# Optimization experiments

Measured on AMD Instinct MI355X. Metric: run time of the kernel, lower is better.

## Reference

```python
import jax, jax.numpy as jnp
import numpy as np

N_HEAD = 16

def setup_inputs() -> dict:
    key = jax.random.key(0)
    ks = jax.random.split(key, 5)
    B, S, D = 4, 2048, 1024
    return {
        "string": jax.random.normal(ks[0], (B, S, D), dtype=jnp.float32),
        "string_len": jax.random.randint(ks[1], (B,), 1, S + 1),
        "Wqkv": jax.random.normal(ks[2], (D, 3 * D), dtype=jnp.float32) * 0.02,
        "bqkv": jnp.zeros((3 * D,), dtype=jnp.float32),
        "Wo": jax.random.normal(ks[3], (D, D), dtype=jnp.float32) * 0.02,
        "bo": jnp.zeros((D,), dtype=jnp.float32),
    }


def reference(string, string_len, Wqkv, bqkv, Wo, bo):
    B, S, D = string.shape
    H = N_HEAD
    hd = D // H
    x = string @ Wqkv + bqkv                      # [B,S,3D]
    q, k, v = jnp.split(x, 3, axis=-1)
    # split heads -> [B,H,S,hd]
    q = q.reshape(B, S, H, hd).transpose(0, 2, 1, 3)
    k = k.reshape(B, S, H, hd).transpose(0, 2, 1, 3)
    v = v.reshape(B, S, H, hd).transpose(0, 2, 1, 3)
    w = jnp.einsum('bhqd,bhkd->bhqk', q, k) / jnp.sqrt(jnp.float32(hd))
    causal = jnp.tril(jnp.ones((S, S), dtype=bool))  # [S,S]
    w = jnp.where(causal[None, None], w, jnp.float32(-1e9))
    w = jax.nn.softmax(w, axis=-1)
    a = jnp.einsum('bhqk,bhkd->bhqd', w, v)       # [B,H,S,hd]
    a = a.transpose(0, 2, 1, 3).reshape(B, S, D)  # merge heads
    a = a @ Wo + bo
    return a, string_len
```

## Files before the change

### kernel.cpp

```cpp
#include <hip/hip_runtime.h>
#include <stdint.h>

typedef __attribute__((ext_vector_type(8))) short bf16x8;
typedef __attribute__((ext_vector_type(4))) float f32x4;
typedef __attribute__((ext_vector_type(16))) float f32x16;
typedef __attribute__((ext_vector_type(4))) unsigned short u16x4;

static constexpr int Bn = 4, Sn = 2048, Dn = 1024, Hn = 16, HD = 64;
static constexpr int Mrows = Bn * Sn;
static constexpr int D3 = 3 * Dn;

__device__ __forceinline__ unsigned short f2bf(float f) {
  unsigned int u = __float_as_uint(f);
  u += 0x7FFF + ((u >> 16) & 1);
  return (unsigned short)(u >> 16);
}

__device__ __forceinline__ void gload16(const void* gptr, void* lptr) {
  __builtin_amdgcn_global_load_lds(
      (__attribute__((address_space(1))) void*)gptr,
      (__attribute__((address_space(3))) void*)lptr, 16, 0, 0);
}

__device__ __forceinline__ int swz8(int r) { return (r ^ (r >> 3)) & 7; }
__device__ __forceinline__ int swz4(int r) { return (r ^ (r >> 2)) & 3; }

__device__ __forceinline__ float vexp2(float x) {
#if __has_builtin(__builtin_amdgcn_exp2f)
  return __builtin_amdgcn_exp2f(x);
#else
  return exp2f(x);
#endif
}

__device__ __forceinline__ unsigned cvtpk(float lo, float hi) {
  unsigned r;
  asm("v_cvt_pk_bf16_f32 %0, %1, %2" : "=v"(r) : "v"(lo), "v"(hi));
  return r;
}

__device__ __forceinline__ float lanepull(float v, int srclane) {
  return __int_as_float(__builtin_amdgcn_ds_bpermute(srclane * 4, __float_as_int(v)));
}

__global__ void cvt_f32_bf16(const float* __restrict__ in,
                             unsigned short* __restrict__ out, int n) {
  int i = (blockIdx.x * blockDim.x + threadIdx.x) * 4;
  if (i < n) {
    const float4 v = *(const float4*)(in + i);
    u16x4 o;
    o.x = f2bf(v.x); o.y = f2bf(v.y); o.z = f2bf(v.z); o.w = f2bf(v.w);
    *(u16x4*)(out + i) = o;
  }
}

__global__ void transpose_cvt(const float* __restrict__ W,
                              unsigned short* __restrict__ Wt, int K, int N) {
  __shared__ float tile[32][33];
  const int n0 = blockIdx.x * 32, k0 = blockIdx.y * 32;
  const int tx = threadIdx.x, ty = threadIdx.y;
  #pragma unroll
  for (int j = 0; j < 4; j++)
    tile[ty + 8 * j][tx] = W[(size_t)(k0 + ty + 8 * j) * N + n0 + tx];
  __syncthreads();
  #pragma unroll
  for (int j = 0; j < 4; j++)
    Wt[(size_t)(n0 + ty + 8 * j) * K + k0 + tx] = f2bf(tile[tx][ty + 8 * j]);
}

template<bool BF16_OUT>
__global__ __launch_bounds__(256, 2)
void gemm_bt(const unsigned short* __restrict__ A,
             const unsigned short* __restrict__ Bt,
             const float* __restrict__ bias,
             void* __restrict__ Cout, int Mt, int Nt, int Kt) {
  __shared__ __align__(16) unsigned short ldsA[128 * 32];
  __shared__ __align__(16) unsigned short ldsB[128 * 32];
  const int tid  = threadIdx.x;
  const int w    = tid >> 6;
  const int lane = tid & 63;
  const int wr = w >> 1, wc = w & 1;
  const int lrow = lane & 15, lk = lane >> 4;
  const long brow = (long)blockIdx.x * 128;
  const long bcol = (long)blockIdx.y * 128;

  f32x4 acc[4][4] = {};

  const int srow_w = w * 16 + (lane >> 2);
  const int sslot  = lane & 3;

  for (int k0 = 0; k0 < Kt; k0 += 32) {
    __syncthreads();
    #pragma unroll
    for (int i = 0; i < 2; i++) {
      const int r  = i * 64 + srow_w;
      const int ca = sslot ^ swz4(r);
      gload16(A  + (size_t)(brow + r) * Kt + k0 + ca * 8, ldsA + i * 2048 + w * 512);
      gload16(Bt + (size_t)(bcol + r) * Kt + k0 + ca * 8, ldsB + i * 2048 + w * 512);
    }
    __syncthreads();
    bf16x8 af[4], bfv[4];
    #pragma unroll
    for (int mt = 0; mt < 4; mt++) {
      const int rr = wr * 64 + mt * 16 + lrow;
      af[mt] = *(const bf16x8*)(ldsA + rr * 32 + ((lk ^ swz4(rr)) * 8));
    }
    #pragma unroll
    for (int nt = 0; nt < 4; nt++) {
      const int rr = wc * 64 + nt * 16 + lrow;
      bfv[nt] = *(const bf16x8*)(ldsB + rr * 32 + ((lk ^ swz4(rr)) * 8));
    }
    #pragma unroll
    for (int mt = 0; mt < 4; mt++)
      #pragma unroll
      for (int nt = 0; nt < 4; nt++)
        acc[mt][nt] = __builtin_amdgcn_mfma_f32_16x16x32_bf16(af[mt], bfv[nt], acc[mt][nt], 0, 0, 0);
  }

  #pragma unroll
  for (int nt = 0; nt < 4; nt++) {
    const long col = bcol + wc * 64 + nt * 16 + lrow;
    const float bv = bias[col];
    #pragma unroll
    for (int mt = 0; mt < 4; mt++) {
      #pragma unroll
      for (int r = 0; r < 4; r++) {
        const long row = brow + wr * 64 + mt * 16 + lk * 4 + r;
        const float v = acc[mt][nt][r] + bv;
        if (BF16_OUT)
          ((unsigned short*)Cout)[row * Nt + col] = f2bf(v);
        else
          ((float*)Cout)[row * Nt + col] = v;
      }
    }
  }
}

__global__ __launch_bounds__(512, 2)
void attn_fwd2(const unsigned short* __restrict__ QKV,
               unsigned short* __restrict__ Out) {
  __shared__ __align__(128) unsigned char smem[65536];
  const int tid  = threadIdx.x;
  const int w    = tid >> 6;
  const int lane = tid & 63;
  const int li = lane & 31, hi = lane >> 5;
  const int bh = blockIdx.x;
  const int b  = bh >> 4, h = bh & 15;
  const int pb = blockIdx.y;
  const int qs = (w < 4) ? (63 - 4 * pb - w) : (4 * pb + (w - 4));
  const int wq = qs * 32;
  const int qrow = wq + li;

  bf16x8 qf[4];
  {
    const unsigned short* qp = QKV + (size_t)(b * Sn + qrow) * D3 + h * HD + hi * 8;
    #pragma unroll
    for (int ks = 0; ks < 4; ks++) qf[ks] = *(const bf16x8*)(qp + ks * 16);
  }

  f32x16 o0 = {}, o1 = {};
  float m = -3.0e38f, lsum = 0.f;
  const float cexp = 0.18033688011112042f;

  auto kstage = [&](int kb, unsigned char* Kb) {
    #pragma unroll
    for (int i = 0; i < 2; i++) {
      const int r    = w * 16 + i * 8 + (lane >> 3);
      const int slot = (lane & 7) ^ swz8(r);
      gload16(QKV + (size_t)(b * Sn + kb + r) * D3 + Dn + h * HD + slot * 8,
              Kb + w * 2048 + i * 1024);
    }
  };
  const int vkv8 = tid >> 3;
  const int vd0  = (tid & 7) * 8;
  auto vload = [&](int kb, int i) -> bf16x8 {
    return *(const bf16x8*)(QKV + (size_t)(b * Sn + kb + i * 64 + vkv8) * D3 + 2 * Dn + h * HD + vd0);
  };
  auto vwrite = [&](bf16x8 vv, int i, unsigned char* Vb) {
    const int kv = i * 64 + vkv8;
    #pragma unroll
    for (int j = 0; j < 8; j++) {
      const int d  = vd0 + j;
      const int vs = (d ^ (d >> 3)) & 15;
      *(unsigned short*)(Vb + d * 256 + (((kv >> 3) ^ vs) << 4) + (kv & 7) * 2) = (unsigned short)vv[j];
    }
  };

  auto substep = [&](int s, int kb, const unsigned char* Kb, const unsigned char* Vb) {
    f32x16 s0 = {}, s1 = {};
    const int r0 = s * 64 + li, r1 = s * 64 + 32 + li;
    __builtin_amdgcn_s_setprio(1);
    #pragma unroll
    for (int ks = 0; ks < 4; ks++) {
      const int slot = ks * 2 + hi;
      const bf16x8 k0 = *(const bf16x8*)(Kb + r0 * 128 + ((slot ^ swz8(r0)) * 16));
      const bf16x8 k1 = *(const bf16x8*)(Kb + r1 * 128 + ((slot ^ swz8(r1)) * 16));
      s0 = __builtin_amdgcn_mfma_f32_32x32x16_bf16(k0, qf[ks], s0, 0, 0, 0);
      s1 = __builtin_amdgcn_mfma_f32_32x32x16_bf16(k1, qf[ks], s1, 0, 0, 0);
    }
    __builtin_amdgcn_s_setprio(0);
    const int kbase = kb + s * 64;
    if (kbase + 63 > wq) {
      #pragma unroll
      for (int r = 0; r < 16; r++) {
        const int kvl = (r & 3) + 8 * (r >> 2) + 4 * hi;
        if (kbase + kvl > qrow)      s0[r] = -3.0e38f;
        if (kbase + 32 + kvl > qrow) s1[r] = -3.0e38f;
      }
    }
    float t8[8];
    #pragma unroll
    for (int r = 0; r < 8; r++)
      t8[r] = fmaxf(fmaxf(s0[r], s0[r + 8]), fmaxf(s1[r], s1[r + 8]));
    float tmax = fmaxf(fmaxf(fmaxf(t8[0], t8[1]), fmaxf(t8[2], t8[3])),
                       fmaxf(fmaxf(t8[4], t8[5]), fmaxf(t8[6], t8[7])));
    tmax = fmaxf(tmax, __shfl_xor(tmax, 32));
    if (__any(tmax > m + 44.0f)) {
      const float mn   = fmaxf(m, tmax);
      const float corr = vexp2((m - mn) * cexp);
      m = mn;
      lsum *= corr;
      #pragma unroll
      for (int r = 0; r < 16; r++) {
        const float cr = lanepull(corr, (r & 3) + 8 * (r >> 2) + 4 * hi);
        o0[r] *= cr; o1[r] *= cr;
      }
    }
    const float mc = m * cexp;
    f32x16 p0, p1;
    float psa = 0.f, psb = 0.f, psc = 0.f, psd = 0.f;
    #pragma unroll
    for (int r = 0; r < 16; r += 4) {
      p0[r] = vexp2(fmaf(s0[r], cexp, -mc));         psa += p0[r];
      p0[r + 1] = vexp2(fmaf(s0[r + 1], cexp, -mc)); psb += p0[r + 1];
      p0[r + 2] = vexp2(fmaf(s0[r + 2], cexp, -mc)); psc += p0[r + 2];
      p0[r + 3] = vexp2(fmaf(s0[r + 3], cexp, -mc)); psd += p0[r + 3];
    }
    #pragma unroll
    for (int r = 0; r < 16; r += 4) {
      p1[r] = vexp2(fmaf(s1[r], cexp, -mc));         psa += p1[r];
      p1[r + 1] = vexp2(fmaf(s1[r + 1], cexp, -mc)); psb += p1[r + 1];
      p1[r + 2] = vexp2(fmaf(s1[r + 2], cexp, -mc)); psc += p1[r + 2];
      p1[r + 3] = vexp2(fmaf(s1[r + 3], cexp, -mc)); psd += p1[r + 3];
    }
    lsum += (psa + psb) + (psc + psd);

    auto mk_pa = [&](const f32x16& pp, int base) -> bf16x8 {
      const unsigned a0 = cvtpk(pp[base + 0], pp[base + 1]);
      const unsigned a1 = cvtpk(pp[base + 2], pp[base + 3]);
      const unsigned b0 = cvtpk(pp[base + 4], pp[base + 5]);
      const unsigned b1 = cvtpk(pp[base + 6], pp[base + 7]);
      const unsigned xa0 = __shfl_xor(a0, 32), xa1 = __shfl_xor(a1, 32);
      const unsigned xb0 = __shfl_xor(b0, 32), xb1 = __shfl_xor(b1, 32);
      union { unsigned u[4]; bf16x8 v; } pu;
      pu.u[0] = hi ? xb0 : a0;
      pu.u[1] = hi ? xb1 : a1;
      pu.u[2] = hi ? b0  : xa0;
      pu.u[3] = hi ? b1  : xa1;
      return pu.v;
    };
    bf16x8 pa[4];
    pa[0] = mk_pa(p0, 0); pa[1] = mk_pa(p0, 8);
    pa[2] = mk_pa(p1, 0); pa[3] = mk_pa(p1, 8);

    const int vs0 = (li ^ (li >> 3)) & 15;
    const int vs1 = ((32 + li) ^ ((32 + li) >> 3)) & 15;
    __builtin_amdgcn_s_setprio(1);
    #pragma unroll
    for (int k16 = 0; k16 < 4; k16++) {
      const int slot = s * 8 + k16 * 2 + hi;
      const bf16x8 vb0 = *(const bf16x8*)(Vb + li * 256 + ((slot ^ vs0) << 4));
      const bf16x8 vb1 = *(const bf16x8*)(Vb + (32 + li) * 256 + ((slot ^ vs1) << 4));
      o0 = __builtin_amdgcn_mfma_f32_32x32x16_bf16(pa[k16], vb0, o0, 0, 0, 0);
      o1 = __builtin_amdgcn_mfma_f32_32x32x16_bf16(pa[k16], vb1, o1, 0, 0, 0);
    }
    __builtin_amdgcn_s_setprio(0);
  };

  kstage(0, smem);
  {
    bf16x8 va = vload(0, 0), vb = vload(0, 1);
    vwrite(va, 0, smem + 16384);
    vwrite(vb, 1, smem + 16384);
  }
  asm volatile("s_waitcnt lgkmcnt(0)");
  __builtin_amdgcn_sched_barrier(0);

  const int qsH = 63 - 4 * pb;
  const int nt  = ((qsH * 32 + 31) >> 7) + 1;
  for (int t = 0; t < nt; t++) {
    const int kb  = t << 7;
    const int cur = t & 1;
    unsigned char* Kb = smem + cur * 32768;
    unsigned char* Vb = Kb + 16384;
    const bool pre = (t + 1 < nt);
    bf16x8 vna, vnb;

    __builtin_amdgcn_s_barrier();
    if (pre) {
      kstage(kb + 128, smem + (cur ^ 1) * 32768);
      vna = vload(kb + 128, 0);
      vnb = vload(kb + 128, 1);
    }

    if (kb <= wq + 31) {
      substep(0, kb, Kb, Vb);
      if (kb + 64 <= wq + 31) substep(1, kb, Kb, Vb);
    }

    if (pre) {
      unsigned char* Vn = smem + (cur ^ 1) * 32768 + 16384;
      vwrite(vna, 0, Vn);
      vwrite(vnb, 1, Vn);
    }
    asm volatile("s_waitcnt lgkmcnt(0)");
    __builtin_amdgcn_sched_barrier(0);
  }

  const float lt = lsum + __shfl_xor(lsum, 32);
  const float rl = __builtin_amdgcn_rcpf(lt);
  #pragma unroll
  for (int r = 0; r < 16; r++) {
    const int q = (r & 3) + 8 * (r >> 2) + 4 * hi;
    const float rr = lanepull(rl, q);
    unsigned short* op = Out + (size_t)(b * Sn + wq + q) * Dn + h * HD;
    op[li]      = f2bf(o0[r] * rr);
    op[32 + li] = f2bf(o1[r] * rr);
  }
}

__global__ void copy_len(const int* __restrict__ slen, float* __restrict__ dst, int n) {
  const int i = threadIdx.x;
  if (i < n) dst[i] = (float)slen[i];
}

extern "C" void kernel_launch(void* const* d_in, const int* in_sizes, int n_in,
                              void* d_out, int out_size, void* d_ws, size_t ws_size,
                              hipStream_t stream) {
  const float* X    = (const float*)d_in[0];
  const int*   slen = (const int*)d_in[1];
  const float* Wqkv = (const float*)d_in[2];
  const float* bqkv = (const float*)d_in[3];
  const float* Wo   = (const float*)d_in[4];
  const float* bo   = (const float*)d_in[5];
  float* out = (float*)d_out;

  char* ws = (char*)d_ws;
  unsigned short* Xb    = (unsigned short*)ws;
  unsigned short* Wtq   = (unsigned short*)(ws + 16777216);
  unsigned short* Wto   = (unsigned short*)(ws + 16777216 + 6291456);
  unsigned short* QKVb  = (unsigned short*)(ws + 16777216 + 6291456 + 2097152);
  unsigned short* Attnb = Xb;

  cvt_f32_bf16<<<dim3(8192), dim3(256), 0, stream>>>(X, Xb, Mrows * Dn);
  transpose_cvt<<<dim3(96, 32), dim3(32, 8), 0, stream>>>(Wqkv, Wtq, Dn, D3);
  transpose_cvt<<<dim3(32, 32), dim3(32, 8), 0, stream>>>(Wo, Wto, Dn, Dn);

  gemm_bt<true><<<dim3(64, 24), dim3(256), 0, stream>>>(Xb, Wtq, bqkv, (void*)QKVb, Mrows, D3, Dn);
  attn_fwd2<<<dim3(64, 8), dim3(512), 0, stream>>>(QKVb, Attnb);
  gemm_bt<false><<<dim3(64, 8), dim3(256), 0, stream>>>(Attnb, Wto, bo, d_out, Mrows, Dn, Dn);
  copy_len<<<dim3(1), dim3(64), 0, stream>>>(slen, out + (size_t)Mrows * Dn, Bn);
}
```

Measured before the change: 189.1 us.

## Rewrite GEMM with 128x256 tiles, K=64 steps and double-buffered LDS prefetch

Replaces the GEMM kernel with a 512-thread version that computes 128x256 output tiles, steps K by 64 per iteration, and double-buffers LDS so the next tile's global-to-LDS load overlaps the current MFMA work. It uses an 8-way XOR swizzle, partial vmcnt waits and s_setprio around the MFMA block. The aim is to hide global load latency and cut the number of barriers per K step. In exchange, 96KB of LDS per block limits occupancy to one block per CU, and the Wo GEMM launches only 256 blocks.

Measured after the change: 188.5 us. Within noise of the previous version (-0.3%).

```diff
diff --git a/kernel.cpp b/kernel.cpp
--- a/kernel.cpp
+++ b/kernel.cpp
@@ -23,7 +23,6 @@
 }
 
 __device__ __forceinline__ int swz8(int r) { return (r ^ (r >> 3)) & 7; }
-__device__ __forceinline__ int swz4(int r) { return (r ^ (r >> 2)) & 3; }
 
 __device__ __forceinline__ float vexp2(float x) {
 #if __has_builtin(__builtin_amdgcn_exp2f)
@@ -69,64 +68,95 @@
 }
 
 template<bool BF16_OUT>
-__global__ __launch_bounds__(256, 2)
-void gemm_bt(const unsigned short* __restrict__ A,
-             const unsigned short* __restrict__ Bt,
-             const float* __restrict__ bias,
-             void* __restrict__ Cout, int Mt, int Nt, int Kt) {
-  __shared__ __align__(16) unsigned short ldsA[128 * 32];
-  __shared__ __align__(16) unsigned short ldsB[128 * 32];
-  const int tid  = threadIdx.x;
-  const int w    = tid >> 6;
-  const int lane = tid & 63;
-  const int wr = w >> 1, wc = w & 1;
+__global__ __launch_bounds__(512, 1)
+void gemm_bt2(const unsigned short* __restrict__ A,
+              const unsigned short* __restrict__ Bt,
+              const float* __restrict__ bias,
+              void* __restrict__ Cout, int Nt, int Kt) {
+  __shared__ __align__(128) unsigned char smem[98304];
+  const int tid = threadIdx.x;
+  const int w = tid >> 6, lane = tid & 63;
+  const int wm = w >> 2, wn = w & 3;
   const int lrow = lane & 15, lk = lane >> 4;
   const long brow = (long)blockIdx.x * 128;
-  const long bcol = (long)blockIdx.y * 128;
+  const long bcol = (long)blockIdx.y * 256;
+
+  const int srow = tid >> 3;
+  const int sslot = tid & 7;
+
+  auto stage = [&](int k0, unsigned char* buf) {
+    unsigned char* Ab = buf;
+    unsigned char* Bb = buf + 16384;
+    #pragma unroll
+    for (int i = 0; i < 2; i++) {
+      const int r = srow + 64 * i;
+      gload16(A + (size_t)(brow + r) * Kt + k0 + ((sslot ^ swz8(r)) * 8),
+              Ab + w * 1024 + i * 8192);
+    }
+    #pragma unroll
+    for (int i = 0; i < 4; i++) {
+      const int r = srow + 64 * i;
+      gload16(Bt + (size_t)(bcol + r) * Kt + k0 + ((sslot ^ swz8(r)) * 8),
+              Bb + w * 1024 + i * 8192);
+    }
+  };
 
   f32x4 acc[4][4] = {};
 
-  const int srow_w = w * 16 + (lane >> 2);
-  const int sslot  = lane & 3;
-
-  for (int k0 = 0; k0 < Kt; k0 += 32) {
-    __syncthreads();
-    #pragma unroll
-    for (int i = 0; i < 2; i++) {
-      const int r  = i * 64 + srow_w;
-      const int ca = sslot ^ swz4(r);
-      gload16(A  + (size_t)(brow + r) * Kt + k0 + ca * 8, ldsA + i * 2048 + w * 512);
-      gload16(Bt + (size_t)(bcol + r) * Kt + k0 + ca * 8, ldsB + i * 2048 + w * 512);
-    }
-    __syncthreads();
-    bf16x8 af[4], bfv[4];
+  stage(0, smem);
+
+  const int ntile = Kt >> 6;
+  for (int t = 0; t < ntile; t++) {
+    const int cur = t & 1;
+    unsigned char* Ab = smem + cur * 49152;
+    unsigned char* Bb = Ab + 16384;
+
+    __builtin_amdgcn_s_barrier();
+    if (t + 1 < ntile) {
+      stage((t + 1) << 6, smem + (cur ^ 1) * 49152);
+      asm volatile("s_waitcnt vmcnt(6)");
+    } else {
+      asm volatile("s_waitcnt vmcnt(0)");
+    }
+    __builtin_amdgcn_sched_barrier(0);
+    __builtin_amdgcn_s_barrier();
+
+    bf16x8 af[4][2], bfv[4][2];
     #pragma unroll
     for (int mt = 0; mt < 4; mt++) {
-      const int rr = wr * 64 + mt * 16 + lrow;
-      af[mt] = *(const bf16x8*)(ldsA + rr * 32 + ((lk ^ swz4(rr)) * 8));
+      const int r = wm * 64 + mt * 16 + lrow;
+      #pragma unroll
+      for (int kk = 0; kk < 2; kk++)
+        af[mt][kk] = *(const bf16x8*)(Ab + r * 128 + (((kk * 4 + lk) ^ swz8(r)) * 16));
     }
     #pragma unroll
     for (int nt = 0; nt < 4; nt++) {
-      const int rr = wc * 64 + nt * 16 + lrow;
-      bfv[nt] = *(const bf16x8*)(ldsB + rr * 32 + ((lk ^ swz4(rr)) * 8));
-    }
+      const int r = wn * 64 + nt * 16 + lrow;
+      #pragma unroll
+      for (int kk = 0; kk < 2; kk++)
+        bfv[nt][kk] = *(const bf16x8*)(Bb + r * 128 + (((kk * 4 + lk) ^ swz8(r)) * 16));
+    }
+    __builtin_amdgcn_s_setprio(1);
     #pragma unroll
     for (int mt = 0; mt < 4; mt++)
       #pragma unroll
-      for (int nt = 0; nt < 4; nt++)
-        acc[mt][nt] = __builtin_amdgcn_mfma_f32_16x16x32_bf16(af[mt], bfv[nt], acc[mt][nt], 0, 0, 0);
+      for (int nt = 0; nt < 4; nt++) {
+        acc[mt][nt] = __builtin_amdgcn_mfma_f32_16x16x32_bf16(af[mt][0], bfv[nt][0], acc[mt][nt], 0, 0, 0);
+        acc[mt][nt] = __builtin_amdgcn_mfma_f32_16x16x32_bf16(af[mt][1], bfv[nt][1], acc[mt][nt], 0, 0, 0);
+      }
+    __builtin_amdgcn_s_setprio(0);
   }
 
   #pragma unroll
   for (int nt = 0; nt < 4; nt++) {
-    const long col = bcol + wc * 64 + nt * 16 + lrow;
+    const long col = bcol + wn * 64 + nt * 16 + lrow;
     const float bv = bias[col];
     #pragma unroll
     for (int mt = 0; mt < 4; mt++) {
       #pragma unroll
-      for (int r = 0; r < 4; r++) {
-        const long row = brow + wr * 64 + mt * 16 + lk * 4 + r;
-        const float v = acc[mt][nt][r] + bv;
+      for (int rr = 0; rr < 4; rr++) {
+        const long row = brow + wm * 64 + mt * 16 + lk * 4 + rr;
+        const float v = acc[mt][nt][rr] + bv;
         if (BF16_OUT)
           ((unsigned short*)Cout)[row * Nt + col] = f2bf(v);
         else
@@ -356,8 +386,8 @@
   transpose_cvt<<<dim3(96, 32), dim3(32, 8), 0, stream>>>(Wqkv, Wtq, Dn, D3);
   transpose_cvt<<<dim3(32, 32), dim3(32, 8), 0, stream>>>(Wo, Wto, Dn, Dn);
 
-  gemm_bt<true><<<dim3(64, 24), dim3(256), 0, stream>>>(Xb, Wtq, bqkv, (void*)QKVb, Mrows, D3, Dn);
+  gemm_bt2<true><<<dim3(64, 12), dim3(512), 0, stream>>>(Xb, Wtq, bqkv, (void*)QKVb, D3, Dn);
   attn_fwd2<<<dim3(64, 8), dim3(512), 0, stream>>>(QKVb, Attnb);
-  gemm_bt<false><<<dim3(64, 8), dim3(256), 0, stream>>>(Attnb, Wto, bo, d_out, Mrows, Dn, Dn);
+  gemm_bt2<false><<<dim3(64, 4), dim3(512), 0, stream>>>(Attnb, Wto, bo, d_out, Dn, Dn);
   copy_len<<<dim3(1), dim3(64), 0, stream>>>(slen, out + (size_t)Mrows * Dn, Bn);
 }
```
